# Optimization experiments

Hardware: AMD Instinct MI355X
Metric: run time of the kernel (lower is better)

The kernel has to match this reference:

```python
import jax, jax.numpy as jnp
import numpy as np

B, OBS, A, T, E, H = 2048, 1024, 512, 64, 16, 64


def setup_inputs() -> dict:
    key = jax.random.key(0)
    ks = jax.random.split(key, 20)
    w = lambda k, shp, s=0.05: (jax.random.normal(k, shp, dtype=jnp.float32) * s)
    x = jax.random.normal(ks[0], (B, OBS), dtype=jnp.float32)
    action_types = jax.random.randint(ks[1], (B, A), 0, T, dtype=jnp.int32)
    # valid action counts in [1, A] so no env has an empty (all -inf) logit row
    action_counts = jax.random.randint(ks[2], (B,), 1, A + 1, dtype=jnp.int32)
    # sampled action must index a valid (unmasked) logit
    action = jnp.mod(jax.random.randint(ks[3], (B,), 0, A, dtype=jnp.int32), action_counts)
    return {
        "x": x, "action_types": action_types, "action_counts": action_counts, "action": action,
        "emb": w(ks[4], (T, E)),
        # actor_base: obs->64->64, tanh
        "W1": w(ks[5], (OBS, H)), "b1": jnp.zeros((H,), jnp.float32),
        "W2": w(ks[6], (H, H)), "b2": jnp.zeros((H,), jnp.float32),
        # action_head first linear split: [feat(64) | embed(16)] -> 64
        "Wf": w(ks[7], (H, H)), "We": w(ks[8], (E, H)), "ba": jnp.zeros((H,), jnp.float32),
        "Wo": w(ks[9], (H, 1), 0.01), "bo": jnp.zeros((1,), jnp.float32),
        # critic: obs->64->64->1, tanh
        "Wc1": w(ks[10], (OBS, H)), "bc1": jnp.zeros((H,), jnp.float32),
        "Wc2": w(ks[11], (H, H)), "bc2": jnp.zeros((H,), jnp.float32),
        "Wc3": w(ks[12], (H, 1), 1.0), "bc3": jnp.zeros((1,), jnp.float32),
    }


def reference(x, action_types, action_counts, action, emb, W1, b1, W2, b2,
              Wf, We, ba, Wo, bo, Wc1, bc1, Wc2, bc2, Wc3, bc3):
    # actor_base features [B,H]
    feats = jnp.tanh(jnp.tanh(x @ W1 + b1) @ W2 + b2)
    # ragged action scoring, padded to [B,A]:
    # combined = cat(feats_broadcast, embed(action_types)); first linear split as Wf/We
    ae = emb[action_types]                                   # [B,A,E]
    h = jnp.tanh((feats @ Wf)[:, None, :] + jnp.einsum('bae,eh->bah', ae, We) + ba)  # [B,A,H]
    scores = jnp.einsum('bah,h->ba', h, Wo[:, 0]) + bo[0]    # [B,A]
    mask = jnp.arange(A, dtype=jnp.int32)[None, :] < action_counts[:, None]
    logits = jnp.where(mask, scores, -jnp.inf)
    logp = jax.nn.log_softmax(logits, axis=-1)               # [B,A]
    log_prob = jnp.take_along_axis(logp, action[:, None].astype(jnp.int32), axis=1)[:, 0]
    p = jnp.exp(logp)
    entropy = -jnp.sum(jnp.where(mask, p * logp, 0.0), axis=-1)
    # critic value [B,1]
    value = jnp.tanh(jnp.tanh(x @ Wc1 + bc1) @ Wc2 + bc2) @ Wc3 + bc3
    return jnp.stack([log_prob, entropy, value[:, 0]], axis=-1)  # [B,3]
```

## Files before the change

### kernel.cpp

```cpp
#include <hip/hip_runtime.h>
#include <hip/hip_bf16.h>

#define B_    2048
#define OBS_  1024
#define A_    512
#define NC    128

typedef __attribute__((ext_vector_type(8))) short bf16x8;
typedef __attribute__((ext_vector_type(4))) float f32x4;

__device__ __forceinline__ float fast_tanh(float x) {
    return 1.0f - 2.0f / (__expf(2.0f * x) + 1.0f);
}

__device__ __forceinline__ unsigned short rne_bf16(float f) {
    union { float f; unsigned u; } v; v.f = f;
    unsigned u = v.u;
    return (unsigned short)((u + 0x7FFFu + ((u >> 16) & 1u)) >> 16);
}

__device__ __forceinline__ unsigned pack_bf16(float lo, float hi) {
    return (unsigned)rne_bf16(lo) | ((unsigned)rne_bf16(hi) << 16);
}

__device__ __forceinline__ short to_bf16(float f) {
    __hip_bfloat16 h = __float2bfloat16(f);
    return *reinterpret_cast<short*>(&h);
}

#define RL(x, k) __int_as_float(__builtin_amdgcn_readlane(__float_as_int(x), (k)))

__global__ __launch_bounds__(256) void k0_prep(
        const float* __restrict__ W1, const float* __restrict__ Wc1,
        const float* __restrict__ emb, const float* __restrict__ We,
        unsigned short* __restrict__ Wfrag, float* __restrict__ embWeT) {
    const int bid = blockIdx.x, tid = threadIdx.x;
    if (bid < 512) {
        int gid   = bid * 256 + tid;
        int i     = gid & 7;
        int lane  = (gid >> 3) & 63;
        int ntile = (gid >> 9) & 7;
        int ks    = gid >> 12;
        int k = ks * 32 + ((lane >> 4) << 3) + i;
        int n = ntile * 16 + (lane & 15);
        float w = (n < 64) ? W1[(size_t)k * 64 + n] : Wc1[(size_t)k * 64 + (n - 64)];
        Wfrag[gid] = rne_bf16(w);
    } else {
        int idx = (bid - 512) * 256 + tid;
        int h = idx >> 6, t = idx & 63;
        float s = 0.f;
        #pragma unroll
        for (int e = 0; e < 16; ++e) s += emb[t * 16 + e] * We[e * 64 + h];
        embWeT[idx] = s;
    }
}

__global__ __launch_bounds__(256) void k1_mfma(
        const float* __restrict__ x, const unsigned short* __restrict__ Wfrag,
        float* __restrict__ partials) {
    const int tid = threadIdx.x;
    const int w   = tid >> 6;
    const int l   = tid & 63;
    const int mb     = blockIdx.x >> 2;
    const int kslice = blockIdx.x & 3;

    const int row  = mb * 16 + (l & 15);
    const int kgrp = (l >> 4) << 3;
    const float* xrow = x + (size_t)row * OBS_ + kslice * 256;
    const bf16x8* Wf8 = (const bf16x8*)Wfrag;

    f32x4 acc0 = {0.f, 0.f, 0.f, 0.f};
    f32x4 acc1 = {0.f, 0.f, 0.f, 0.f};
    const int nt0 = w * 2, nt1 = w * 2 + 1;

    #pragma unroll
    for (int ks = 0; ks < 8; ++ks) {
        const float4* xp = (const float4*)(xrow + ks * 32 + kgrp);
        float4 a0 = xp[0];
        float4 a1 = xp[1];
        bf16x8 av;
        av[0] = to_bf16(a0.x); av[1] = to_bf16(a0.y);
        av[2] = to_bf16(a0.z); av[3] = to_bf16(a0.w);
        av[4] = to_bf16(a1.x); av[5] = to_bf16(a1.y);
        av[6] = to_bf16(a1.z); av[7] = to_bf16(a1.w);
        const int kg = kslice * 8 + ks;
        bf16x8 bv0 = Wf8[(kg * 8 + nt0) * 64 + l];
        bf16x8 bv1 = Wf8[(kg * 8 + nt1) * 64 + l];
        acc0 = __builtin_amdgcn_mfma_f32_16x16x32_bf16(av, bv0, acc0, 0, 0, 0);
        acc1 = __builtin_amdgcn_mfma_f32_16x16x32_bf16(av, bv1, acc1, 0, 0, 0);
    }

    float* pbase = partials + (size_t)kslice * B_ * NC;
    const int rbase = mb * 16 + ((l >> 4) << 2);
    {
        int col = nt0 * 16 + (l & 15);
        #pragma unroll
        for (int r = 0; r < 4; ++r)
            pbase[(size_t)(rbase + r) * NC + col] = acc0[r];
    }
    {
        int col = nt1 * 16 + (l & 15);
        #pragma unroll
        for (int r = 0; r < 4; ++r)
            pbase[(size_t)(rbase + r) * NC + col] = acc1[r];
    }
}

__global__ __launch_bounds__(256) void k2_score(
        const float* __restrict__ partials, const float* __restrict__ embWeT,
        const int* __restrict__ action_types, const int* __restrict__ action_counts,
        const int* __restrict__ action,
        const float* __restrict__ b1, const float* __restrict__ bc1,
        const float* __restrict__ W2, const float* __restrict__ b2,
        const float* __restrict__ Wf,
        const float* __restrict__ ba, const float* __restrict__ Wo,
        const float* __restrict__ bo, const float* __restrict__ Wc2,
        const float* __restrict__ bc2, const float* __restrict__ Wc3,
        const float* __restrict__ bc3, float* __restrict__ out) {
    __shared__ unsigned sW2p[32][64];
    __shared__ unsigned sWfp[32][64];
    __shared__ unsigned sWc2p[32][64];
    __shared__ unsigned sVTp[32][64];
    __shared__ int scnt[4][64];

    const int tid = threadIdx.x;
    #pragma unroll
    for (int i = 0; i < 8; ++i) {
        int idx = tid + i * 256;
        int rp = idx >> 6, hh = idx & 63;
        sW2p [rp][hh] = pack_bf16(W2 [(2 * rp) * 64 + hh], W2 [(2 * rp + 1) * 64 + hh]);
        sWfp [rp][hh] = pack_bf16(Wf [(2 * rp) * 64 + hh], Wf [(2 * rp + 1) * 64 + hh]);
        sWc2p[rp][hh] = pack_bf16(Wc2[(2 * rp) * 64 + hh], Wc2[(2 * rp + 1) * 64 + hh]);
        sVTp [rp][hh] = pack_bf16(embWeT[(2 * rp) * 64 + hh], embWeT[(2 * rp + 1) * 64 + hh]);
    }
    scnt[tid >> 6][tid & 63] = 0;
    __syncthreads();

    const int lane = tid & 63;
    const int wid  = tid >> 6;
    const int b    = blockIdx.x * 4 + wid;

    const float* pa = partials + (size_t)b * NC + lane;
    const float* pc = pa + 64;
    float h1v = pa[0] + pa[1 * B_ * NC] + pa[2 * B_ * NC] + pa[3 * B_ * NC];
    float c1v = pc[0] + pc[1 * B_ * NC] + pc[2 * B_ * NC] + pc[3 * B_ * NC];
    h1v = fast_tanh(h1v + b1[lane]);
    c1v = fast_tanh(c1v + bc1[lane]);
    const int* at_row = action_types + (size_t)b * A_;
    const int count = action_counts[b];
    const int base = lane * 8;
    int4 p0 = *reinterpret_cast<const int4*>(at_row + base);
    int4 p1 = *reinterpret_cast<const int4*>(at_row + base + 4);
    const int a_star = action[b];
    const int t_star = at_row[a_star] & 63;

    float f = b2[lane];
    #pragma unroll
    for (int kp = 0; kp < 32; ++kp) {
        unsigned pw = sW2p[kp][lane];
        f += RL(h1v, 2 * kp)     * __uint_as_float(pw << 16);
        f += RL(h1v, 2 * kp + 1) * __uint_as_float(pw & 0xffff0000u);
    }
    f = fast_tanh(f);

    float u = ba[lane];
    #pragma unroll
    for (int kp = 0; kp < 32; ++kp) {
        unsigned pw = sWfp[kp][lane];
        u += RL(f, 2 * kp)     * __uint_as_float(pw << 16);
        u += RL(f, 2 * kp + 1) * __uint_as_float(pw & 0xffff0000u);
    }

    float cc = bc2[lane];
    #pragma unroll
    for (int kp = 0; kp < 32; ++kp) {
        unsigned pw = sWc2p[kp][lane];
        cc += RL(c1v, 2 * kp)     * __uint_as_float(pw << 16);
        cc += RL(c1v, 2 * kp + 1) * __uint_as_float(pw & 0xffff0000u);
    }
    cc = fast_tanh(cc);
    float pv = cc * Wc3[lane];
    #pragma unroll
    for (int off = 32; off > 0; off >>= 1) pv += __shfl_xor(pv, off);
    const float value = pv + bc3[0];

    float s = bo[0];
    #pragma unroll
    for (int hp = 0; hp < 32; ++hp) {
        unsigned pvv = sVTp[hp][lane];
        s += fast_tanh(RL(u, 2 * hp)     + __uint_as_float(pvv << 16))         * Wo[2 * hp];
        s += fast_tanh(RL(u, 2 * hp + 1) + __uint_as_float(pvv & 0xffff0000u)) * Wo[2 * hp + 1];
    }

    int* cptr = scnt[wid];
    if (base + 0 < count) atomicAdd(&cptr[p0.x & 63], 1);
    if (base + 1 < count) atomicAdd(&cptr[p0.y & 63], 1);
    if (base + 2 < count) atomicAdd(&cptr[p0.z & 63], 1);
    if (base + 3 < count) atomicAdd(&cptr[p0.w & 63], 1);
    if (base + 4 < count) atomicAdd(&cptr[p1.x & 63], 1);
    if (base + 5 < count) atomicAdd(&cptr[p1.y & 63], 1);
    if (base + 6 < count) atomicAdd(&cptr[p1.z & 63], 1);
    if (base + 7 < count) atomicAdd(&cptr[p1.w & 63], 1);

    const int cv = cptr[lane];
    float mval = (cv > 0) ? s : -3.0e38f;
    #pragma unroll
    for (int off = 32; off > 0; off >>= 1) mval = fmaxf(mval, __shfl_xor(mval, off));
    const float e  = (float)cv * __expf(s - mval);
    float se = e, sd = e * s;
    #pragma unroll
    for (int off = 32; off > 0; off >>= 1) {
        se += __shfl_xor(se, off);
        sd += __shfl_xor(sd, off);
    }
    const float logZ    = mval + __logf(se);
    const float entropy = logZ - sd / se;
    const float logp    = __shfl(s, t_star) - logZ;

    if (lane == 0) {
        out[b * 3 + 0] = logp;
        out[b * 3 + 1] = entropy;
        out[b * 3 + 2] = value;
    }
}

extern "C" void kernel_launch(void* const* d_in, const int* in_sizes, int n_in,
                              void* d_out, int out_size, void* d_ws, size_t ws_size,
                              hipStream_t stream) {
    const float* x             = (const float*)d_in[0];
    const int*   action_types  = (const int*)  d_in[1];
    const int*   action_counts = (const int*)  d_in[2];
    const int*   action        = (const int*)  d_in[3];
    const float* emb           = (const float*)d_in[4];
    const float* W1            = (const float*)d_in[5];
    const float* b1            = (const float*)d_in[6];
    const float* W2            = (const float*)d_in[7];
    const float* b2            = (const float*)d_in[8];
    const float* Wf            = (const float*)d_in[9];
    const float* We            = (const float*)d_in[10];
    const float* ba            = (const float*)d_in[11];
    const float* Wo            = (const float*)d_in[12];
    const float* bo            = (const float*)d_in[13];
    const float* Wc1           = (const float*)d_in[14];
    const float* bc1           = (const float*)d_in[15];
    const float* Wc2           = (const float*)d_in[16];
    const float* bc2           = (const float*)d_in[17];
    const float* Wc3           = (const float*)d_in[18];
    const float* bc3           = (const float*)d_in[19];
    float* out = (float*)d_out;

    unsigned char* ws = (unsigned char*)d_ws;
    unsigned short* Wfrag  = (unsigned short*)ws;
    float*          embWeT = (float*)(ws + 262144);
    float*          partials = (float*)(ws + 262144 + 16384);

    k0_prep<<<528, 256, 0, stream>>>(W1, Wc1, emb, We, Wfrag, embWeT);
    k1_mfma<<<512, 256, 0, stream>>>(x, Wfrag, partials);
    k2_score<<<512, 256, 0, stream>>>(partials, embWeT, action_types, action_counts,
                                      action, b1, bc1, W2, b2, Wf, ba, Wo, bo,
                                      Wc2, bc2, Wc3, bc3, out);
}
```

Measured before the change: 28.88 us.

## Fuse weight prep into MFMA kernel via LDS transpose and split K eight ways

Removes the separate prep kernel. Each MFMA block now reads its 128-row K slice of W1/Wc1, converts it to bf16 and transposes it into padded shared memory, then feeds MFMA B operands from LDS. K is split into 8 slices over 1024 blocks instead of 4 over 512, so partials doubles and the score kernel sums 8 slices. The embWe precompute moves into the first 16 blocks. This saves one launch but makes every block redo the weight conversion and doubles the partials traffic.

```diff
diff --git a/kernel.cpp b/kernel.cpp
--- a/kernel.cpp
+++ b/kernel.cpp
@@ -5,6 +5,8 @@
 #define OBS_  1024
 #define A_    512
 #define NC    128
+#define NSLICE 8
+#define PADK  136
 
 typedef __attribute__((ext_vector_type(8))) short bf16x8;
 typedef __attribute__((ext_vector_type(4))) float f32x4;
@@ -30,52 +32,51 @@
 
 #define RL(x, k) __int_as_float(__builtin_amdgcn_readlane(__float_as_int(x), (k)))
 
-__global__ __launch_bounds__(256) void k0_prep(
-        const float* __restrict__ W1, const float* __restrict__ Wc1,
-        const float* __restrict__ emb, const float* __restrict__ We,
-        unsigned short* __restrict__ Wfrag, float* __restrict__ embWeT) {
-    const int bid = blockIdx.x, tid = threadIdx.x;
-    if (bid < 512) {
-        int gid   = bid * 256 + tid;
-        int i     = gid & 7;
-        int lane  = (gid >> 3) & 63;
-        int ntile = (gid >> 9) & 7;
-        int ks    = gid >> 12;
-        int k = ks * 32 + ((lane >> 4) << 3) + i;
-        int n = ntile * 16 + (lane & 15);
-        float w = (n < 64) ? W1[(size_t)k * 64 + n] : Wc1[(size_t)k * 64 + (n - 64)];
-        Wfrag[gid] = rne_bf16(w);
-    } else {
-        int idx = (bid - 512) * 256 + tid;
-        int h = idx >> 6, t = idx & 63;
-        float s = 0.f;
-        #pragma unroll
-        for (int e = 0; e < 16; ++e) s += emb[t * 16 + e] * We[e * 64 + h];
-        embWeT[idx] = s;
-    }
-}
-
 __global__ __launch_bounds__(256) void k1_mfma(
-        const float* __restrict__ x, const unsigned short* __restrict__ Wfrag,
-        float* __restrict__ partials) {
-    const int tid = threadIdx.x;
-    const int w   = tid >> 6;
-    const int l   = tid & 63;
-    const int mb     = blockIdx.x >> 2;
-    const int kslice = blockIdx.x & 3;
-
-    const int row  = mb * 16 + (l & 15);
-    const int kgrp = (l >> 4) << 3;
-    const float* xrow = x + (size_t)row * OBS_ + kslice * 256;
-    const bf16x8* Wf8 = (const bf16x8*)Wfrag;
+        const float* __restrict__ x, const float* __restrict__ W1,
+        const float* __restrict__ Wc1, const float* __restrict__ emb,
+        const float* __restrict__ We, float* __restrict__ partials,
+        float* __restrict__ embWeT) {
+    __shared__ unsigned short wT[128 * PADK];
+    const int tid    = threadIdx.x;
+    const int mb     = blockIdx.x >> 3;
+    const int kslice = blockIdx.x & 7;
+    const int k0     = kslice * 128;
+
+    {
+        const int n  = tid & 127;
+        const int th = tid >> 7;
+        const float* src = (n < 64) ? (W1 + n) : (Wc1 + (n - 64));
+        #pragma unroll
+        for (int gg = 0; gg < 16; ++gg) {
+            int kq = gg * 2 + th;
+            int k  = k0 + kq * 4;
+            float w0 = src[(size_t)(k + 0) * 64];
+            float w1 = src[(size_t)(k + 1) * 64];
+            float w2 = src[(size_t)(k + 2) * 64];
+            float w3 = src[(size_t)(k + 3) * 64];
+            unsigned long long v = (unsigned long long)pack_bf16(w0, w1)
+                                 | ((unsigned long long)pack_bf16(w2, w3) << 32);
+            *reinterpret_cast<unsigned long long*>(&wT[n * PADK + kq * 4]) = v;
+        }
+    }
+    __syncthreads();
+
+    const int w = tid >> 6;
+    const int l = tid & 63;
+    const int c = l & 15;
+    const int g = l >> 4;
+
+    const float* xrow = x + (size_t)(mb * 16 + c) * OBS_ + k0 + g * 8;
+    const int nt0 = 2 * w, nt1 = 2 * w + 1;
+    const unsigned short* bp0 = &wT[(nt0 * 16 + c) * PADK + g * 8];
+    const unsigned short* bp1 = &wT[(nt1 * 16 + c) * PADK + g * 8];
 
     f32x4 acc0 = {0.f, 0.f, 0.f, 0.f};
     f32x4 acc1 = {0.f, 0.f, 0.f, 0.f};
-    const int nt0 = w * 2, nt1 = w * 2 + 1;
-
-    #pragma unroll
-    for (int ks = 0; ks < 8; ++ks) {
-        const float4* xp = (const float4*)(xrow + ks * 32 + kgrp);
+    #pragma unroll
+    for (int ks = 0; ks < 4; ++ks) {
+        const float4* xp = (const float4*)(xrow + ks * 32);
         float4 a0 = xp[0];
         float4 a1 = xp[1];
         bf16x8 av;
@@ -83,26 +84,34 @@
         av[2] = to_bf16(a0.z); av[3] = to_bf16(a0.w);
         av[4] = to_bf16(a1.x); av[5] = to_bf16(a1.y);
         av[6] = to_bf16(a1.z); av[7] = to_bf16(a1.w);
-        const int kg = kslice * 8 + ks;
-        bf16x8 bv0 = Wf8[(kg * 8 + nt0) * 64 + l];
-        bf16x8 bv1 = Wf8[(kg * 8 + nt1) * 64 + l];
+        bf16x8 bv0 = *(const bf16x8*)(bp0 + ks * 32);
+        bf16x8 bv1 = *(const bf16x8*)(bp1 + ks * 32);
         acc0 = __builtin_amdgcn_mfma_f32_16x16x32_bf16(av, bv0, acc0, 0, 0, 0);
         acc1 = __builtin_amdgcn_mfma_f32_16x16x32_bf16(av, bv1, acc1, 0, 0, 0);
     }
 
     float* pbase = partials + (size_t)kslice * B_ * NC;
-    const int rbase = mb * 16 + ((l >> 4) << 2);
+    const int rbase = mb * 16 + g * 4;
     {
-        int col = nt0 * 16 + (l & 15);
+        int col = nt0 * 16 + c;
         #pragma unroll
         for (int r = 0; r < 4; ++r)
             pbase[(size_t)(rbase + r) * NC + col] = acc0[r];
     }
     {
-        int col = nt1 * 16 + (l & 15);
+        int col = nt1 * 16 + c;
         #pragma unroll
         for (int r = 0; r < 4; ++r)
             pbase[(size_t)(rbase + r) * NC + col] = acc1[r];
+    }
+
+    if (blockIdx.x < 16) {
+        int idx = blockIdx.x * 256 + tid;
+        int h = idx >> 6, t = idx & 63;
+        float s = 0.f;
+        #pragma unroll
+        for (int e = 0; e < 16; ++e) s += emb[t * 16 + e] * We[e * 64 + h];
+        embWeT[idx] = s;
     }
 }
 
@@ -141,9 +150,12 @@
     const int b    = blockIdx.x * 4 + wid;
 
     const float* pa = partials + (size_t)b * NC + lane;
-    const float* pc = pa + 64;
-    float h1v = pa[0] + pa[1 * B_ * NC] + pa[2 * B_ * NC] + pa[3 * B_ * NC];
-    float c1v = pc[0] + pc[1 * B_ * NC] + pc[2 * B_ * NC] + pc[3 * B_ * NC];
+    float h1v = 0.f, c1v = 0.f;
+    #pragma unroll
+    for (int s8 = 0; s8 < NSLICE; ++s8) {
+        h1v += pa[(size_t)s8 * B_ * NC];
+        c1v += pa[(size_t)s8 * B_ * NC + 64];
+    }
     h1v = fast_tanh(h1v + b1[lane]);
     c1v = fast_tanh(c1v + bc1[lane]);
     const int* at_row = action_types + (size_t)b * A_;
@@ -250,12 +262,10 @@
     float* out = (float*)d_out;
 
     unsigned char* ws = (unsigned char*)d_ws;
-    unsigned short* Wfrag  = (unsigned short*)ws;
-    float*          embWeT = (float*)(ws + 262144);
-    float*          partials = (float*)(ws + 262144 + 16384);
-
-    k0_prep<<<528, 256, 0, stream>>>(W1, Wc1, emb, We, Wfrag, embWeT);
-    k1_mfma<<<512, 256, 0, stream>>>(x, Wfrag, partials);
+    float* embWeT   = (float*)ws;
+    float* partials = (float*)(ws + 16384);
+
+    k1_mfma<<<1024, 256, 0, stream>>>(x, W1, Wc1, emb, We, partials, embWeT);
     k2_score<<<512, 256, 0, stream>>>(partials, embWeT, action_types, action_counts,
                                       action, b1, bc1, W2, b2, Wf, ba, Wo, bo,
                                       Wc2, bc2, Wc3, bc3, out);
```

Measured after the change: 28.04 us. 2.9% less time.
